# Kernel optimization log

Measured on AMD Instinct MI355X. Metric: run time of the kernel, lower is better.

## Reference

```python
import jax, jax.numpy as jnp
import numpy as np
import math

BATCH, SEQ, D_CONTENT = 16, 512, 1024
D_POSITION, NUM_TILES, D_HIDDEN = 64, 8, 4096


def _make_pe(max_len, d_model):
    pe = np.zeros((max_len, d_model), dtype=np.float32)
    position = np.arange(max_len, dtype=np.float32)[:, None]
    div_term = np.exp(np.arange(0, d_model, 2, dtype=np.float32) * (-math.log(10000.0) / d_model))
    pe[:, 0::2] = np.sin(position * div_term)
    pe[:, 1::2] = np.cos(position * div_term)
    return jnp.asarray(pe)


def setup_inputs() -> dict:
    key = jax.random.key(0)
    ks = jax.random.split(key, 8)
    x = jax.random.normal(ks[0], (BATCH, SEQ, D_CONTENT), dtype=jnp.float32)
    pe = _make_pe(SEQ, D_POSITION)  # (SEQ, D_POSITION), buffer sliced to seq len
    position_weight = jnp.asarray(0.5, dtype=jnp.float32)
    content_weight = jnp.asarray(0.5, dtype=jnp.float32)
    pos_sigs = jax.random.normal(ks[1], (NUM_TILES, D_POSITION), dtype=jnp.float32)
    content_sigs = jax.random.normal(ks[2], (NUM_TILES, D_CONTENT), dtype=jnp.float32)
    s1 = 1.0 / math.sqrt(D_CONTENT)
    s2 = 1.0 / math.sqrt(D_HIDDEN)
    W1 = jax.random.normal(ks[3], (NUM_TILES, D_CONTENT, D_HIDDEN), dtype=jnp.float32) * s1
    b1 = jax.random.normal(ks[4], (NUM_TILES, D_HIDDEN), dtype=jnp.float32) * s1
    W2 = jax.random.normal(ks[5], (NUM_TILES, D_HIDDEN, D_CONTENT), dtype=jnp.float32) * s2
    b2 = jax.random.normal(ks[6], (NUM_TILES, D_CONTENT), dtype=jnp.float32) * s2
    return {"x": x, "pe": pe, "position_weight": position_weight,
            "content_weight": content_weight, "pos_sigs": pos_sigs,
            "content_sigs": content_sigs, "W1": W1, "b1": b1, "W2": W2, "b2": b2}


def reference(x, pe, position_weight, content_weight, pos_sigs, content_sigs, W1, b1, W2, b2):
    B, S, _ = x.shape
    num_tiles = W1.shape[0]
    # normalized position/content mixing weights
    pw = jax.nn.sigmoid(position_weight)
    cw = jax.nn.sigmoid(content_weight)
    tot = pw + cw
    pw, cw = pw / tot, cw / tot
    # mixed address: [pw * pos_enc | cw * x] -> (B, S, Dp + Dc)
    pos_part = jnp.broadcast_to((pw * pe[:S])[None], (B, S, pe.shape[-1]))
    address = jnp.concatenate([pos_part, cw * x], axis=-1)
    # ternarized signatures (T, Dp + Dc)
    signatures = jnp.concatenate([jnp.sign(pos_sigs), jnp.sign(content_sigs)], axis=-1)
    scores = jnp.einsum('bsd,td->bst', address, signatures)
    indices = jnp.argmax(scores, axis=-1)  # (B, S) top-1 tile per token
    # dispatch: per-tile gelu MLP, combined via top-1 mask (loop over fixed small tile count)
    out = jnp.zeros_like(x)
    for t in range(num_tiles):
        h = jax.nn.gelu(jnp.einsum('bsd,dh->bsh', x, W1[t]) + b1[t], approximate=False)
        y = jnp.einsum('bsh,hd->bsd', h, W2[t]) + b2[t]
        out = out + jnp.where((indices == t)[..., None], y, jnp.zeros((), x.dtype))
    return out
```

## Files before the change

### kernel.cpp

```cpp
#include <hip/hip_runtime.h>
#include <hip/hip_bf16.h>
#include <math.h>

#define BATCH 16
#define SEQ   512
#define DC    1024
#define DP    64
#define NT    8
#define DH    4096
#define NTOK  (BATCH*SEQ)

#define BM 128
#define BN 128
#define BK 32

typedef __attribute__((ext_vector_type(8))) short short8;
typedef __attribute__((ext_vector_type(4))) float floatx4;
typedef __attribute__((ext_vector_type(4))) unsigned short ushort4v;
typedef __attribute__((ext_vector_type(8))) unsigned short ushort8v;

__device__ __forceinline__ unsigned short f2bf(float f) {
  union { float f; unsigned u; } v; v.f = f;
  unsigned r = v.u + 0x7FFFu + ((v.u >> 16) & 1u);
  return (unsigned short)(r >> 16);
}

__device__ __forceinline__ void gl_lds16(const void* g, void* l) {
  __builtin_amdgcn_global_load_lds(
      (__attribute__((address_space(1))) void*)g,
      (__attribute__((address_space(3))) void*)l, 16, 0, 0);
}

__global__ __launch_bounds__(256) void route_kernel(
    const float* __restrict__ x, const float* __restrict__ pe,
    const float* __restrict__ pwp, const float* __restrict__ cwp,
    const float* __restrict__ pos_sigs, const float* __restrict__ csigs,
    int* __restrict__ counts, int* __restrict__ list,
    unsigned short* __restrict__ xb) {
  int wid  = threadIdx.x >> 6;
  int lane = threadIdx.x & 63;
  int token = blockIdx.x * 4 + wid;
  int s = token & (SEQ - 1);

  float pwr = 1.f / (1.f + expf(-pwp[0]));
  float cwr = 1.f / (1.f + expf(-cwp[0]));
  float tot = pwr + cwr;
  float pw = pwr / tot, cw = cwr / tot;

  float acc[NT];
#pragma unroll
  for (int t = 0; t < NT; t++) acc[t] = 0.f;

  float a0 = pw * pe[s * DP + lane];
#pragma unroll
  for (int t = 0; t < NT; t++) {
    float v = pos_sigs[t * DP + lane];
    float sg = (v > 0.f) ? 1.f : ((v < 0.f) ? -1.f : 0.f);
    acc[t] = fmaf(a0, sg, acc[t]);
  }

  const float* xrow = x + (size_t)token * DC;
  unsigned short* xbrow = xb + (size_t)token * DC;
#pragma unroll 4
  for (int i = 0; i < DC / 64; i++) {
    int c = lane + i * 64;
    float xv = xrow[c];
    xbrow[c] = f2bf(xv);
    float a = cw * xv;
#pragma unroll
    for (int t = 0; t < NT; t++) {
      float v = csigs[t * DC + c];
      float sg = (v > 0.f) ? 1.f : ((v < 0.f) ? -1.f : 0.f);
      acc[t] = fmaf(a, sg, acc[t]);
    }
  }

#pragma unroll
  for (int off = 32; off >= 1; off >>= 1)
#pragma unroll
    for (int t = 0; t < NT; t++) acc[t] += __shfl_xor(acc[t], off);

  if (lane == 0) {
    int best = 0; float bv = acc[0];
#pragma unroll
    for (int t = 1; t < NT; t++)
      if (acc[t] > bv) { bv = acc[t]; best = t; }
    int slot = atomicAdd(&counts[best], 1);
    list[best * NTOK + slot] = token;
  }
}

template<int AR, int AC>
__global__ __launch_bounds__(256) void transpose_kernel(
    const float* __restrict__ in, unsigned short* __restrict__ out) {
  __shared__ unsigned short tile[64 * 65];
  int t = blockIdx.z;
  const float* in_t = in + (size_t)t * AR * AC;
  unsigned short* out_t = out + (size_t)t * AR * AC;
  int x0 = blockIdx.x * 64, y0 = blockIdx.y * 64;
  int tid = threadIdx.x;
  int ry = tid >> 2, cx = (tid & 3) * 16;
  const float* src = in_t + (size_t)(y0 + ry) * AC + x0 + cx;
  float4 v0 = *(const float4*)(src);
  float4 v1 = *(const float4*)(src + 4);
  float4 v2 = *(const float4*)(src + 8);
  float4 v3 = *(const float4*)(src + 12);
  unsigned short* trow = &tile[ry * 65 + cx];
  trow[0]  = f2bf(v0.x); trow[1]  = f2bf(v0.y); trow[2]  = f2bf(v0.z); trow[3]  = f2bf(v0.w);
  trow[4]  = f2bf(v1.x); trow[5]  = f2bf(v1.y); trow[6]  = f2bf(v1.z); trow[7]  = f2bf(v1.w);
  trow[8]  = f2bf(v2.x); trow[9]  = f2bf(v2.y); trow[10] = f2bf(v2.z); trow[11] = f2bf(v2.w);
  trow[12] = f2bf(v3.x); trow[13] = f2bf(v3.y); trow[14] = f2bf(v3.z); trow[15] = f2bf(v3.w);
  __syncthreads();
  int rx = tid >> 2, cy = (tid & 3) * 16;
  ushort8v o0, o1;
#pragma unroll
  for (int j = 0; j < 8; j++) o0[j] = tile[(cy + j) * 65 + rx];
#pragma unroll
  for (int j = 0; j < 8; j++) o1[j] = tile[(cy + 8 + j) * 65 + rx];
  size_t ob = (size_t)(x0 + rx) * AR + y0 + cy;
  *(ushort8v*)&out_t[ob]     = o0;
  *(ushort8v*)&out_t[ob + 8] = o1;
}

template<int K, int N, bool GELU>
__global__ __launch_bounds__(256) void gemm_async_kernel(
    const unsigned short* __restrict__ A, const unsigned short* __restrict__ BT,
    const float* __restrict__ bias, const int* __restrict__ counts,
    const int* __restrict__ list, unsigned short* __restrict__ Hout,
    float* __restrict__ Fout) {
  int t = blockIdx.z;
  int count = counts[t];
  int base = blockIdx.y * BM;
  if (base >= count) return;
  int j0 = blockIdx.x * BN;

  __shared__ unsigned short As[BM * BK];
  __shared__ unsigned short Bs[BN * BK];
  __shared__ int toks[BM];

  int tid = threadIdx.x;
  if (tid < BM) {
    int slot = base + tid;
    toks[tid] = (slot < count) ? list[t * NTOK + slot] : -1;
  }
  __syncthreads();

  int w = tid >> 6, lane = tid & 63;
  int lrow = lane >> 2;
  int lc   = lane & 3;
  int swz  = (lc ^ ((lrow >> 1) & 3)) * 8;

  const unsigned short* srcA[2];
  const unsigned short* srcB[2];
  unsigned short* dstA[2];
  unsigned short* dstB[2];
#pragma unroll
  for (int i = 0; i < 2; i++) {
    int ch = i * 4 + w;
    int r = ch * 16 + lrow;
    int tk = toks[r]; if (tk < 0) tk = 0;
    srcA[i] = A + (size_t)tk * K + swz;
    srcB[i] = BT + (size_t)t * N * K + (size_t)(j0 + r) * K + swz;
    dstA[i] = &As[ch * 512];
    dstB[i] = &Bs[ch * 512];
  }

  int wm = (w & 1) * 64, wn = (w >> 1) * 64;
  int quad = lane >> 4, l15 = lane & 15;
  int fswz = (quad ^ ((l15 >> 1) & 3)) * 8;

  floatx4 acc[4][4];
#pragma unroll
  for (int mi = 0; mi < 4; mi++)
#pragma unroll
    for (int ni = 0; ni < 4; ni++) acc[mi][ni] = (floatx4){0.f, 0.f, 0.f, 0.f};

  for (int k0 = 0; k0 < K; k0 += BK) {
#pragma unroll
    for (int i = 0; i < 2; i++) {
      gl_lds16(srcA[i], dstA[i]);
      gl_lds16(srcB[i], dstB[i]);
      srcA[i] += BK; srcB[i] += BK;
    }
    __syncthreads();

    short8 a[4], b[4];
#pragma unroll
    for (int mi = 0; mi < 4; mi++)
      a[mi] = *(const short8*)&As[(wm + mi * 16 + l15) * BK + fswz];
#pragma unroll
    for (int ni = 0; ni < 4; ni++)
      b[ni] = *(const short8*)&Bs[(wn + ni * 16 + l15) * BK + fswz];
#pragma unroll
    for (int mi = 0; mi < 4; mi++)
#pragma unroll
      for (int ni = 0; ni < 4; ni++)
        acc[mi][ni] = __builtin_amdgcn_mfma_f32_16x16x32_bf16(a[mi], b[ni], acc[mi][ni], 0, 0, 0);
    __syncthreads();
  }

#pragma unroll
  for (int ni = 0; ni < 4; ni++) {
    int n = j0 + wn + ni * 16 + l15;
    float bv = bias[t * N + n];
#pragma unroll
    for (int mi = 0; mi < 4; mi++) {
      int mb = wm + mi * 16 + quad * 4;
#pragma unroll
      for (int r = 0; r < 4; r++) {
        int tok = toks[mb + r];
        if (tok >= 0) {
          float v = acc[mi][ni][r] + bv;
          if (GELU) {
            v = 0.5f * v * (1.f + erff(v * 0.70710678118654752f));
            Hout[(size_t)tok * N + n] = f2bf(v);
          } else {
            Fout[(size_t)tok * N + n] = v;
          }
        }
      }
    }
  }
}

template<int K, int N, bool GELU>
__global__ __launch_bounds__(256) void gemm_pipe_kernel(
    const unsigned short* __restrict__ A, const unsigned short* __restrict__ BT,
    const float* __restrict__ bias, const int* __restrict__ counts,
    const int* __restrict__ list, unsigned short* __restrict__ Hout,
    float* __restrict__ Fout) {
  int t = blockIdx.z;
  int count = counts[t];
  int base = blockIdx.y * BM;
  if (base >= count) return;
  int j0 = blockIdx.x * BN;

  __shared__ __align__(16) unsigned short As[3][BM * BK];
  __shared__ __align__(16) unsigned short Bs[3][BN * BK];
  __shared__ int toks[BM];

  int tid = threadIdx.x;
  if (tid < BM) {
    int slot = base + tid;
    toks[tid] = (slot < count) ? list[t * NTOK + slot] : -1;
  }
  __syncthreads();

  int w = tid >> 6, lane = tid & 63;
  int lrow = lane >> 2;
  int lc   = lane & 3;
  int swz  = (lc ^ ((lrow >> 1) & 3)) * 8;

  const unsigned short* srcA[2];
  const unsigned short* srcB[2];
  int cho[2];
#pragma unroll
  for (int i = 0; i < 2; i++) {
    int ch = i * 4 + w;
    int r = ch * 16 + lrow;
    int tk = toks[r]; if (tk < 0) tk = 0;
    srcA[i] = A + (size_t)tk * K + swz;
    srcB[i] = BT + (size_t)t * N * K + (size_t)(j0 + r) * K + swz;
    cho[i] = ch * 512;
  }

  int wm = (w & 1) * 64, wn = (w >> 1) * 64;
  int quad = lane >> 4, l15 = lane & 15;
  int fswz = (quad ^ ((l15 >> 1) & 3)) * 8;

  floatx4 acc[4][4];
#pragma unroll
  for (int mi = 0; mi < 4; mi++)
#pragma unroll
    for (int ni = 0; ni < 4; ni++) acc[mi][ni] = (floatx4){0.f, 0.f, 0.f, 0.f};

  constexpr int S = K / BK;
  unsigned short *a0 = As[0], *a1 = As[1], *a2 = As[2];
  unsigned short *b0 = Bs[0], *b1 = Bs[1], *b2 = Bs[2];

#pragma unroll
  for (int i = 0; i < 2; i++) {
    gl_lds16(srcA[i], a0 + cho[i]); gl_lds16(srcB[i], b0 + cho[i]);
    srcA[i] += BK; srcB[i] += BK;
  }
#pragma unroll
  for (int i = 0; i < 2; i++) {
    gl_lds16(srcA[i], a1 + cho[i]); gl_lds16(srcB[i], b1 + cho[i]);
    srcA[i] += BK; srcB[i] += BK;
  }
  asm volatile("s_waitcnt vmcnt(4)" ::: "memory");
  __builtin_amdgcn_s_barrier();

#pragma unroll 1
  for (int k = 0; k < S - 1; ++k) {
    short8 a[4], b[4];
#pragma unroll
    for (int mi = 0; mi < 4; mi++)
      a[mi] = *(const short8*)&a0[(wm + mi * 16 + l15) * BK + fswz];
#pragma unroll
    for (int ni = 0; ni < 4; ni++)
      b[ni] = *(const short8*)&b0[(wn + ni * 16 + l15) * BK + fswz];

    if (k < S - 2) {
#pragma unroll
      for (int i = 0; i < 2; i++) {
        gl_lds16(srcA[i], a2 + cho[i]); gl_lds16(srcB[i], b2 + cho[i]);
        srcA[i] += BK; srcB[i] += BK;
      }
    }

    __builtin_amdgcn_s_setprio(1);
#pragma unroll
    for (int mi = 0; mi < 4; mi++)
#pragma unroll
      for (int ni = 0; ni < 4; ni++)
        acc[mi][ni] = __builtin_amdgcn_mfma_f32_16x16x32_bf16(a[mi], b[ni], acc[mi][ni], 0, 0, 0);
    __builtin_amdgcn_s_setprio(0);

    if (k < S - 2) {
      asm volatile("s_waitcnt vmcnt(4)" ::: "memory");
    } else {
      asm volatile("s_waitcnt vmcnt(0)" ::: "memory");
    }
    __builtin_amdgcn_s_barrier();

    unsigned short* tp;
    tp = a0; a0 = a1; a1 = a2; a2 = tp;
    tp = b0; b0 = b1; b1 = b2; b2 = tp;
  }

  {
    short8 a[4], b[4];
#pragma unroll
    for (int mi = 0; mi < 4; mi++)
      a[mi] = *(const short8*)&a0[(wm + mi * 16 + l15) * BK + fswz];
#pragma unroll
    for (int ni = 0; ni < 4; ni++)
      b[ni] = *(const short8*)&b0[(wn + ni * 16 + l15) * BK + fswz];
#pragma unroll
    for (int mi = 0; mi < 4; mi++)
#pragma unroll
      for (int ni = 0; ni < 4; ni++)
        acc[mi][ni] = __builtin_amdgcn_mfma_f32_16x16x32_bf16(a[mi], b[ni], acc[mi][ni], 0, 0, 0);
  }

#pragma unroll
  for (int ni = 0; ni < 4; ni++) {
    int n = j0 + wn + ni * 16 + l15;
    float bv = bias[t * N + n];
#pragma unroll
    for (int mi = 0; mi < 4; mi++) {
      int mb = wm + mi * 16 + quad * 4;
#pragma unroll
      for (int r = 0; r < 4; r++) {
        int tok = toks[mb + r];
        if (tok >= 0) {
          float v = acc[mi][ni][r] + bv;
          if (GELU) {
            v = 0.5f * v * (1.f + erff(v * 0.70710678118654752f));
            Hout[(size_t)tok * N + n] = f2bf(v);
          } else {
            Fout[(size_t)tok * N + n] = v;
          }
        }
      }
    }
  }
}

#define KPAD 40
__global__ __launch_bounds__(256) void gemm1_fb(
    const unsigned short* __restrict__ xb, const float* __restrict__ W1,
    const float* __restrict__ b1, const int* __restrict__ counts,
    const int* __restrict__ list, unsigned short* __restrict__ H) {
  int t = blockIdx.z;
  int count = counts[t];
  int base = blockIdx.y * BM;
  if (base >= count) return;
  int j0 = blockIdx.x * BN;
  __shared__ unsigned short As[BM][KPAD];
  __shared__ unsigned short Bs[BN][KPAD];
  __shared__ int toks[BM];
  int tid = threadIdx.x;
  if (tid < BM) {
    int slot = base + tid;
    toks[tid] = (slot < count) ? list[t * NTOK + slot] : -1;
  }
  __syncthreads();
  int arow = tid >> 1, acol = (tid & 1) * 16;
  int mytok = toks[arow];
  const unsigned short* xrow = xb + (size_t)(mytok < 0 ? 0 : mytok) * DC;
  int kg4 = (tid >> 5) * 4, ng4 = (tid & 31) * 4;
  const float* Wt = W1 + (size_t)t * DC * DH;
  int wid = tid >> 6, lane = tid & 63;
  int wm = (wid & 1) * 64, wn = (wid >> 1) * 64;
  int quad = lane >> 4, l15 = lane & 15;
  floatx4 acc[4][4];
#pragma unroll
  for (int mi = 0; mi < 4; mi++)
#pragma unroll
    for (int ni = 0; ni < 4; ni++) acc[mi][ni] = (floatx4){0.f, 0.f, 0.f, 0.f};
  for (int kt = 0; kt < DC / BK; kt++) {
    int k0 = kt * BK;
    if (mytok >= 0) {
      *(uint4*)&As[arow][acol]     = *(const uint4*)(xrow + k0 + acol);
      *(uint4*)&As[arow][acol + 8] = *(const uint4*)(xrow + k0 + acol + 8);
    } else {
      uint4 z = {0u,0u,0u,0u};
      *(uint4*)&As[arow][acol] = z; *(uint4*)&As[arow][acol + 8] = z;
    }
    const float* wb = Wt + (size_t)(k0 + kg4) * DH + j0 + ng4;
    float4 r0 = *(const float4*)(wb);
    float4 r1 = *(const float4*)(wb + DH);
    float4 r2 = *(const float4*)(wb + 2 * DH);
    float4 r3 = *(const float4*)(wb + 3 * DH);
    ushort4v c0 = { f2bf(r0.x), f2bf(r1.x), f2bf(r2.x), f2bf(r3.x) };
    ushort4v c1 = { f2bf(r0.y), f2bf(r1.y), f2bf(r2.y), f2bf(r3.y) };
    ushort4v c2 = { f2bf(r0.z), f2bf(r1.z), f2bf(r2.z), f2bf(r3.z) };
    ushort4v c3 = { f2bf(r0.w), f2bf(r1.w), f2bf(r2.w), f2bf(r3.w) };
    *(ushort4v*)&Bs[ng4 + 0][kg4] = c0; *(ushort4v*)&Bs[ng4 + 1][kg4] = c1;
    *(ushort4v*)&Bs[ng4 + 2][kg4] = c2; *(ushort4v*)&Bs[ng4 + 3][kg4] = c3;
    __syncthreads();
    short8 a[4], b[4];
#pragma unroll
    for (int mi = 0; mi < 4; mi++) a[mi] = *(const short8*)&As[wm + mi * 16 + l15][quad * 8];
#pragma unroll
    for (int ni = 0; ni < 4; ni++) b[ni] = *(const short8*)&Bs[wn + ni * 16 + l15][quad * 8];
#pragma unroll
    for (int mi = 0; mi < 4; mi++)
#pragma unroll
      for (int ni = 0; ni < 4; ni++)
        acc[mi][ni] = __builtin_amdgcn_mfma_f32_16x16x32_bf16(a[mi], b[ni], acc[mi][ni], 0, 0, 0);
    __syncthreads();
  }
#pragma unroll
  for (int ni = 0; ni < 4; ni++) {
    int n = j0 + wn + ni * 16 + l15;
    float bias = b1[t * DH + n];
#pragma unroll
    for (int mi = 0; mi < 4; mi++) {
      int mb = wm + mi * 16 + quad * 4;
#pragma unroll
      for (int r = 0; r < 4; r++) {
        int tok = toks[mb + r];
        if (tok >= 0) {
          float v = acc[mi][ni][r] + bias;
          v = 0.5f * v * (1.f + erff(v * 0.70710678118654752f));
          H[(size_t)tok * DH + n] = f2bf(v);
        }
      }
    }
  }
}

__global__ __launch_bounds__(256) void gemm2_fb(
    const unsigned short* __restrict__ H, const float* __restrict__ W2,
    const float* __restrict__ b2, const int* __restrict__ counts,
    const int* __restrict__ list, float* __restrict__ out) {
  int t = blockIdx.z;
  int count = counts[t];
  int base = blockIdx.y * BM;
  if (base >= count) return;
  int j0 = blockIdx.x * BN;
  __shared__ unsigned short As[BM][KPAD];
  __shared__ unsigned short Bs[BN][KPAD];
  __shared__ int toks[BM];
  int tid = threadIdx.x;
  if (tid < BM) {
    int slot = base + tid;
    toks[tid] = (slot < count) ? list[t * NTOK + slot] : -1;
  }
  __syncthreads();
  int arow = tid >> 1, acol = (tid & 1) * 16;
  int mytok = toks[arow];
  const unsigned short* hrow = H + (size_t)(mytok < 0 ? 0 : mytok) * DH;
  int kg4 = (tid >> 5) * 4, ng4 = (tid & 31) * 4;
  const float* Wt = W2 + (size_t)t * DH * DC;
  int wid = tid >> 6, lane = tid & 63;
  int wm = (wid & 1) * 64, wn = (wid >> 1) * 64;
  int quad = lane >> 4, l15 = lane & 15;
  floatx4 acc[4][4];
#pragma unroll
  for (int mi = 0; mi < 4; mi++)
#pragma unroll
    for (int ni = 0; ni < 4; ni++) acc[mi][ni] = (floatx4){0.f, 0.f, 0.f, 0.f};
  for (int kt = 0; kt < DH / BK; kt++) {
    int k0 = kt * BK;
    if (mytok >= 0) {
      *(uint4*)&As[arow][acol]     = *(const uint4*)(hrow + k0 + acol);
      *(uint4*)&As[arow][acol + 8] = *(const uint4*)(hrow + k0 + acol + 8);
    } else {
      uint4 z = {0u,0u,0u,0u};
      *(uint4*)&As[arow][acol] = z; *(uint4*)&As[arow][acol + 8] = z;
    }
    const float* wb = Wt + (size_t)(k0 + kg4) * DC + j0 + ng4;
    float4 r0 = *(const float4*)(wb);
    float4 r1 = *(const float4*)(wb + DC);
    float4 r2 = *(const float4*)(wb + 2 * DC);
    float4 r3 = *(const float4*)(wb + 3 * DC);
    ushort4v c0 = { f2bf(r0.x), f2bf(r1.x), f2bf(r2.x), f2bf(r3.x) };
    ushort4v c1 = { f2bf(r0.y), f2bf(r1.y), f2bf(r2.y), f2bf(r3.y) };
    ushort4v c2 = { f2bf(r0.z), f2bf(r1.z), f2bf(r2.z), f2bf(r3.z) };
    ushort4v c3 = { f2bf(r0.w), f2bf(r1.w), f2bf(r2.w), f2bf(r3.w) };
    *(ushort4v*)&Bs[ng4 + 0][kg4] = c0; *(ushort4v*)&Bs[ng4 + 1][kg4] = c1;
    *(ushort4v*)&Bs[ng4 + 2][kg4] = c2; *(ushort4v*)&Bs[ng4 + 3][kg4] = c3;
    __syncthreads();
    short8 a[4], b[4];
#pragma unroll
    for (int mi = 0; mi < 4; mi++) a[mi] = *(const short8*)&As[wm + mi * 16 + l15][quad * 8];
#pragma unroll
    for (int ni = 0; ni < 4; ni++) b[ni] = *(const short8*)&Bs[wn + ni * 16 + l15][quad * 8];
#pragma unroll
    for (int mi = 0; mi < 4; mi++)
#pragma unroll
      for (int ni = 0; ni < 4; ni++)
        acc[mi][ni] = __builtin_amdgcn_mfma_f32_16x16x32_bf16(a[mi], b[ni], acc[mi][ni], 0, 0, 0);
    __syncthreads();
  }
#pragma unroll
  for (int ni = 0; ni < 4; ni++) {
    int n = j0 + wn + ni * 16 + l15;
    float bias = b2[t * DC + n];
#pragma unroll
    for (int mi = 0; mi < 4; mi++) {
      int mb = wm + mi * 16 + quad * 4;
#pragma unroll
      for (int r = 0; r < 4; r++) {
        int tok = toks[mb + r];
        if (tok >= 0) out[(size_t)tok * DC + n] = acc[mi][ni][r] + bias;
      }
    }
  }
}

extern "C" void kernel_launch(void* const* d_in, const int* in_sizes, int n_in,
                              void* d_out, int out_size, void* d_ws, size_t ws_size,
                              hipStream_t stream) {
  const float* x        = (const float*)d_in[0];
  const float* pe       = (const float*)d_in[1];
  const float* pwp      = (const float*)d_in[2];
  const float* cwp      = (const float*)d_in[3];
  const float* pos_sigs = (const float*)d_in[4];
  const float* csigs    = (const float*)d_in[5];
  const float* W1       = (const float*)d_in[6];
  const float* b1       = (const float*)d_in[7];
  const float* W2       = (const float*)d_in[8];
  const float* b2       = (const float*)d_in[9];
  float* out = (float*)d_out;

  char* ws = (char*)d_ws;
  int* counts = (int*)ws;
  int* list   = (int*)(ws + 1024);
  unsigned short* xb = (unsigned short*)(ws + (1 << 20));

  hipMemsetAsync(counts, 0, NT * sizeof(int), stream);
  route_kernel<<<NTOK / 4, 256, 0, stream>>>(x, pe, pwp, cwp, pos_sigs, csigs,
                                             counts, list, xb);

  if (ws_size >= (size_t)145 * 1024 * 1024) {
    unsigned short* WT = (unsigned short*)(ws + ((size_t)17 << 20));
    unsigned short* H  = (unsigned short*)(ws + ((size_t)81 << 20));

    transpose_kernel<DC, DH><<<dim3(DH / 64, DC / 64, NT), 256, 0, stream>>>(W1, WT);
    gemm_pipe_kernel<DC, DH, true><<<dim3(DH / BN, NTOK / BM, NT), 256, 0, stream>>>(
        xb, WT, b1, counts, list, H, nullptr);
    transpose_kernel<DH, DC><<<dim3(DC / 64, DH / 64, NT), 256, 0, stream>>>(W2, WT);
    gemm_async_kernel<DH, DC, false><<<dim3(DC / BN, NTOK / BM, NT), 256, 0, stream>>>(
        H, WT, b2, counts, list, nullptr, out);
  } else {
    unsigned short* H = (unsigned short*)(ws + ((size_t)32 << 20));
    gemm1_fb<<<dim3(DH / BN, NTOK / BM, NT), 256, 0, stream>>>(xb, W1, b1, counts, list, H);
    gemm2_fb<<<dim3(DC / BN, NTOK / BM, NT), 256, 0, stream>>>(H, W2, b2, counts, list, out);
  }
}
```

Measured before the change: 699.0 us.

## Triple-buffer GEMM pipelines, interleave tile-major block order, deterministic routing compaction

Routing is split into a scoring kernel that writes each token's best tile and a compaction kernel that uses ballot and prefix sums to build per-tile token lists in order, replacing the atomic append and the memset. GEMM1 now runs on a new 3-stage async LDS pipeline kernel with partial vmcnt waits and MFMA priority raising, in place of the earlier pipe kernel. GEMM2 switches to the 3-stage pipe kernel with a 1D grid where the tile index is the fastest-varying part of the block id, so different experts' blocks are interleaved. The sequential compaction over all tokens in only 8 blocks adds a small serial step.

```diff
diff --git a/kernel.cpp b/kernel.cpp
--- a/kernel.cpp
+++ b/kernel.cpp
@@ -31,12 +31,11 @@
       (__attribute__((address_space(3))) void*)l, 16, 0, 0);
 }
 
-__global__ __launch_bounds__(256) void route_kernel(
+__global__ __launch_bounds__(256) void route_score(
     const float* __restrict__ x, const float* __restrict__ pe,
     const float* __restrict__ pwp, const float* __restrict__ cwp,
     const float* __restrict__ pos_sigs, const float* __restrict__ csigs,
-    int* __restrict__ counts, int* __restrict__ list,
-    unsigned short* __restrict__ xb) {
+    int* __restrict__ best, unsigned short* __restrict__ xb) {
   int wid  = threadIdx.x >> 6;
   int lane = threadIdx.x & 63;
   int token = blockIdx.x * 4 + wid;
@@ -81,13 +80,38 @@
     for (int t = 0; t < NT; t++) acc[t] += __shfl_xor(acc[t], off);
 
   if (lane == 0) {
-    int best = 0; float bv = acc[0];
+    int bt = 0; float bv = acc[0];
 #pragma unroll
     for (int t = 1; t < NT; t++)
-      if (acc[t] > bv) { bv = acc[t]; best = t; }
-    int slot = atomicAdd(&counts[best], 1);
-    list[best * NTOK + slot] = token;
-  }
+      if (acc[t] > bv) { bv = acc[t]; bt = t; }
+    best[token] = bt;
+  }
+}
+
+__global__ __launch_bounds__(256) void route_compact(
+    const int* __restrict__ best, int* __restrict__ counts,
+    int* __restrict__ list) {
+  int t = blockIdx.x;
+  int tid = threadIdx.x;
+  int lane = tid & 63, wid = tid >> 6;
+  __shared__ int wsum[4];
+  int running = 0;
+  for (int base = 0; base < NTOK; base += 256) {
+    int tok = base + tid;
+    bool f = (best[tok] == t);
+    unsigned long long m = __ballot(f);
+    int rank = __popcll(m & ((1ULL << lane) - 1ULL));
+    if (lane == 0) wsum[wid] = __popcll(m);
+    __syncthreads();
+    int wb = 0;
+#pragma unroll
+    for (int i = 0; i < 4; i++) if (i < wid) wb += wsum[i];
+    int ctot = wsum[0] + wsum[1] + wsum[2] + wsum[3];
+    if (f) list[t * NTOK + running + wb + rank] = tok;
+    running += ctot;
+    __syncthreads();
+  }
+  if (tid == 0) counts[t] = running;
 }
 
 template<int AR, int AC>
@@ -123,7 +147,7 @@
 }
 
 template<int K, int N, bool GELU>
-__global__ __launch_bounds__(256) void gemm_async_kernel(
+__global__ __launch_bounds__(256) void gemm_pipe3d_kernel(
     const unsigned short* __restrict__ A, const unsigned short* __restrict__ BT,
     const float* __restrict__ bias, const int* __restrict__ counts,
     const int* __restrict__ list, unsigned short* __restrict__ Hout,
@@ -134,8 +158,8 @@
   if (base >= count) return;
   int j0 = blockIdx.x * BN;
 
-  __shared__ unsigned short As[BM * BK];
-  __shared__ unsigned short Bs[BN * BK];
+  __shared__ __align__(16) unsigned short As[3][BM * BK];
+  __shared__ __align__(16) unsigned short Bs[3][BN * BK];
   __shared__ int toks[BM];
 
   int tid = threadIdx.x;
@@ -152,8 +176,7 @@
 
   const unsigned short* srcA[2];
   const unsigned short* srcB[2];
-  unsigned short* dstA[2];
-  unsigned short* dstB[2];
+  int cho[2];
 #pragma unroll
   for (int i = 0; i < 2; i++) {
     int ch = i * 4 + w;
@@ -161,8 +184,7 @@
     int tk = toks[r]; if (tk < 0) tk = 0;
     srcA[i] = A + (size_t)tk * K + swz;
     srcB[i] = BT + (size_t)t * N * K + (size_t)(j0 + r) * K + swz;
-    dstA[i] = &As[ch * 512];
-    dstB[i] = &Bs[ch * 512];
+    cho[i] = ch * 512;
   }
 
   int wm = (w & 1) * 64, wn = (w >> 1) * 64;
@@ -175,28 +197,74 @@
 #pragma unroll
     for (int ni = 0; ni < 4; ni++) acc[mi][ni] = (floatx4){0.f, 0.f, 0.f, 0.f};
 
-  for (int k0 = 0; k0 < K; k0 += BK) {
-#pragma unroll
-    for (int i = 0; i < 2; i++) {
-      gl_lds16(srcA[i], dstA[i]);
-      gl_lds16(srcB[i], dstB[i]);
-      srcA[i] += BK; srcB[i] += BK;
-    }
-    __syncthreads();
-
+  constexpr int S = K / BK;
+  unsigned short *a0 = As[0], *a1 = As[1], *a2 = As[2];
+  unsigned short *b0 = Bs[0], *b1 = Bs[1], *b2 = Bs[2];
+
+#pragma unroll
+  for (int i = 0; i < 2; i++) {
+    gl_lds16(srcA[i], a0 + cho[i]); gl_lds16(srcB[i], b0 + cho[i]);
+    srcA[i] += BK; srcB[i] += BK;
+  }
+#pragma unroll
+  for (int i = 0; i < 2; i++) {
+    gl_lds16(srcA[i], a1 + cho[i]); gl_lds16(srcB[i], b1 + cho[i]);
+    srcA[i] += BK; srcB[i] += BK;
+  }
+  asm volatile("s_waitcnt vmcnt(4)" ::: "memory");
+  __builtin_amdgcn_s_barrier();
+
+#pragma unroll 1
+  for (int k = 0; k < S - 1; ++k) {
     short8 a[4], b[4];
 #pragma unroll
     for (int mi = 0; mi < 4; mi++)
-      a[mi] = *(const short8*)&As[(wm + mi * 16 + l15) * BK + fswz];
+      a[mi] = *(const short8*)&a0[(wm + mi * 16 + l15) * BK + fswz];
 #pragma unroll
     for (int ni = 0; ni < 4; ni++)
-      b[ni] = *(const short8*)&Bs[(wn + ni * 16 + l15) * BK + fswz];
+      b[ni] = *(const short8*)&b0[(wn + ni * 16 + l15) * BK + fswz];
+
+    if (k < S - 2) {
+#pragma unroll
+      for (int i = 0; i < 2; i++) {
+        gl_lds16(srcA[i], a2 + cho[i]); gl_lds16(srcB[i], b2 + cho[i]);
+        srcA[i] += BK; srcB[i] += BK;
+      }
+    }
+
+    __builtin_amdgcn_s_setprio(1);
 #pragma unroll
     for (int mi = 0; mi < 4; mi++)
 #pragma unroll
       for (int ni = 0; ni < 4; ni++)
         acc[mi][ni] = __builtin_amdgcn_mfma_f32_16x16x32_bf16(a[mi], b[ni], acc[mi][ni], 0, 0, 0);
-    __syncthreads();
+    __builtin_amdgcn_s_setprio(0);
+
+    if (k < S - 2) {
+      asm volatile("s_waitcnt vmcnt(4)" ::: "memory");
+    } else {
+      asm volatile("s_waitcnt vmcnt(0)" ::: "memory");
+    }
+    __builtin_amdgcn_s_barrier();
+
+    unsigned short* tp;
+    tp = a0; a0 = a1; a1 = a2; a2 = tp;
+    tp = b0; b0 = b1; b1 = b2; b2 = tp;
+  }
+
+  {
+    short8 a[4], b[4];
+#pragma unroll
+    for (int mi = 0; mi < 4; mi++)
+      a[mi] = *(const short8*)&a0[(wm + mi * 16 + l15) * BK + fswz];
+#pragma unroll
+    for (int ni = 0; ni < 4; ni++)
+      b[ni] = *(const short8*)&b0[(wn + ni * 16 + l15) * BK + fswz];
+#pragma unroll
+    for (int mi = 0; mi < 4; mi++)
+#pragma unroll
+      for (int ni = 0; ni < 4; ni++)
+        acc[mi][ni] = __builtin_amdgcn_mfma_f32_16x16x32_bf16(a[mi], b[ni], acc[mi][ni], 0, 0, 0);
   }
 
 #pragma unroll
@@ -223,17 +291,22 @@
   }
 }
 
-template<int K, int N, bool GELU>
+template<int K, int N, int NXB, bool GELU>
 __global__ __launch_bounds__(256) void gemm_pipe_kernel(
     const unsigned short* __restrict__ A, const unsigned short* __restrict__ BT,
     const float* __restrict__ bias, const int* __restrict__ counts,
     const int* __restrict__ list, unsigned short* __restrict__ Hout,
     float* __restrict__ Fout) {
-  int t = blockIdx.z;
+  unsigned bid = blockIdx.x;
+  int t = bid & (NT - 1);
+  unsigned inner = bid >> 3;
+  int bx = inner & (NXB - 1);
+  int by = inner / NXB;
+
   int count = counts[t];
-  int base = blockIdx.y * BM;
+  int base = by * BM;
   if (base >= count) return;
-  int j0 = blockIdx.x * BN;
+  int j0 = bx * BN;
 
   __shared__ __align__(16) unsigned short As[3][BM * BK];
   __shared__ __align__(16) unsigned short Bs[3][BN * BK];
@@ -551,21 +624,24 @@
   char* ws = (char*)d_ws;
   int* counts = (int*)ws;
   int* list   = (int*)(ws + 1024);
+  int* best   = (int*)(ws + 300 * 1024);
   unsigned short* xb = (unsigned short*)(ws + (1 << 20));
 
-  hipMemsetAsync(counts, 0, NT * sizeof(int), stream);
-  route_kernel<<<NTOK / 4, 256, 0, stream>>>(x, pe, pwp, cwp, pos_sigs, csigs,
-                                             counts, list, xb);
+  route_score<<<NTOK / 4, 256, 0, stream>>>(x, pe, pwp, cwp, pos_sigs, csigs,
+                                            best, xb);
+  route_compact<<<NT, 256, 0, stream>>>(best, counts, list);
 
   if (ws_size >= (size_t)145 * 1024 * 1024) {
     unsigned short* WT = (unsigned short*)(ws + ((size_t)17 << 20));
     unsigned short* H  = (unsigned short*)(ws + ((size_t)81 << 20));
 
     transpose_kernel<DC, DH><<<dim3(DH / 64, DC / 64, NT), 256, 0, stream>>>(W1, WT);
-    gemm_pipe_kernel<DC, DH, true><<<dim3(DH / BN, NTOK / BM, NT), 256, 0, stream>>>(
+    gemm_pipe3d_kernel<DC, DH, true>
+        <<<dim3(DH / BN, NTOK / BM, NT), 256, 0, stream>>>(
         xb, WT, b1, counts, list, H, nullptr);
     transpose_kernel<DH, DC><<<dim3(DC / 64, DH / 64, NT), 256, 0, stream>>>(W2, WT);
-    gemm_async_kernel<DH, DC, false><<<dim3(DC / BN, NTOK / BM, NT), 256, 0, stream>>>(
+    gemm_pipe_kernel<DH, DC, DC / BN, false>
+        <<<(DC / BN) * (NTOK / BM) * NT, 256, 0, stream>>>(
         H, WT, b2, counts, list, nullptr, out);
   } else {
     unsigned short* H = (unsigned short*)(ws + ((size_t)32 << 20));
```

Measured after the change: 597.8 us. 14.5% less time.
